# Optimization experiments

Measured on AMD Instinct MI355X. Metric: run time of the kernel, lower is better.

## Reference

```python
import jax, jax.numpy as jnp
import numpy as np

B, C, H, W = 2, 32, 128, 128
K = 5            # window_size
NH = 2           # num_heads
HD = C // NH     # head_dim = 16
KK = K * K
HID = int(2 * C * 2.0)  # mlp hidden = dim*2*mlp_ratio = 128
SCALE = HD ** -0.5


def _ln(x, w, b, eps=1e-5):
    m = jnp.mean(x, -1, keepdims=True)
    v = jnp.var(x, -1, keepdims=True)
    return (x - m) * jax.lax.rsqrt(v + eps) * w + b


def _windows(t):
    # t: [B,H,W,C] -> [B,H,W,C,K*K]; zero-padded KxK neighborhood per pixel
    # (same layout as nn.Unfold: kernel position is the fastest-varying axis).
    p = (K - 1) // 2
    Hc, Wc = t.shape[1], t.shape[2]
    tp = jnp.pad(t, ((0, 0), (p, p), (p, p), (0, 0)))
    return jnp.stack([tp[:, i:i + Hc, j:j + Wc, :] for i in range(K) for j in range(K)], axis=-1)


def _rel_index():
    # Swin-style relative position index for a KxK window -> [KK,KK] ints
    c = jnp.stack(jnp.meshgrid(jnp.arange(K), jnp.arange(K), indexing='ij'), 0).reshape(2, -1)
    r = (c[:, :, None] - c[:, None, :]).transpose(1, 2, 0) + (K - 1)
    return r[..., 0] * (2 * K - 1) + r[..., 1]


def _ckbd_mask(h, w):
    # checkerboard attention mask: [L, KK, KK] additive (0 or -100)
    ck = jnp.zeros((h, w), jnp.float32)
    ck = ck.at[0::2, 1::2].set(1.0).at[1::2, 0::2].set(1.0)
    cw = _windows(ck[None, :, :, None])[0, :, :, 0, :].reshape(h * w, KK)  # [L,KK]
    m = cw[:, :, None] * cw[:, None, :]
    return jnp.where(m == 1.0, 0.0, -100.0)


def setup_inputs() -> dict:
    key = jax.random.key(0)
    ks = jax.random.split(key, 8)
    p = lambda k, s: (0.02 * jax.random.normal(k, s)).astype(jnp.float32)
    return dict(
        x=jax.random.normal(ks[0], (B, C, H, W), dtype=jnp.float32),
        qkv_w=p(ks[1], (3 * C, C)), qkv_b=jnp.zeros((3 * C,), jnp.float32),
        rel_table=p(ks[2], ((2 * K - 1) ** 2, NH)),
        norm1_w=jnp.ones((C,), jnp.float32), norm1_b=jnp.zeros((C,), jnp.float32),
        norm2_w=jnp.ones((2 * C,), jnp.float32), norm2_b=jnp.zeros((2 * C,), jnp.float32),
        proj_w=p(ks[3], (2 * C, 2 * C)), proj_b=jnp.zeros((2 * C,), jnp.float32),
        fusion_w=p(ks[4], (2 * C, C, K, K)), fusion_b=jnp.zeros((2 * C,), jnp.float32),
        mlp_w1=p(ks[5], (HID, 2 * C)), mlp_b1=jnp.zeros((HID,), jnp.float32),
        mlp_w2=p(ks[6], (2 * C, HID)), mlp_b2=jnp.zeros((2 * C,), jnp.float32),
    )


def reference(x, qkv_w, qkv_b, rel_table, norm1_w, norm1_b, norm2_w, norm2_b,
              proj_w, proj_b, fusion_w, fusion_b, mlp_w1, mlp_b1, mlp_w2, mlp_b2):
    Bs, Cs, Hs, Ws = x.shape
    L = Hs * Ws
    xt = x.reshape(Bs, Cs, L).transpose(0, 2, 1)          # [B,L,C]
    xn = _ln(xt, norm1_w, norm1_b)
    qkv = jnp.einsum('blc,oc->blo', xn, qkv_w) + qkv_b     # [B,L,3C]
    qkv = qkv.reshape(Bs, Hs, Ws, 3, Cs)
    q, k, v = qkv[..., 0, :], qkv[..., 1, :], qkv[..., 2, :]  # each [B,H,W,C]

    def heads(t):
        # windows -> [B,L,C,KK]; split C as (head_dim, num_heads) to match the
        # original reshape(B,L,head_dim,num_heads,KK).permute(0,1,3,4,2)
        w_ = _windows(t).reshape(Bs, L, HD, NH, KK)
        return w_.transpose(0, 1, 3, 4, 2)                 # [B,L,nh,KK,hd]

    qh, kh, vh = heads(q), heads(k), heads(v)
    attn = jnp.einsum('blhqd,blhkd->blhqk', qh * SCALE, kh)  # [B,L,nh,KK,KK]

    bias = rel_table[_rel_index().reshape(-1)].reshape(KK, KK, NH).transpose(2, 0, 1)
    attn = attn + bias[None, None]
    attn = attn + _ckbd_mask(Hs, Ws)[None, :, None]
    attn = jax.nn.softmax(attn, axis=-1)

    o = jnp.einsum('blhqk,blhkd->blhqd', attn, vh)           # [B,L,nh,KK,hd]
    # -> [B,L,K,K,nh,hd] -> [B,L,K,K,C] (head-major channel order, as in torch)
    o = o.reshape(Bs, L, NH, K, K, HD).transpose(0, 1, 3, 4, 2, 5).reshape(Bs, L, K, K, Cs)
    # fusion: Conv2d(C, 2C, kernel=K) on [BL,C,K,K] with no padding == full contraction
    y = jnp.einsum('blijc,ocij->blo', o, fusion_w) + fusion_b  # [B,L,2C]
    y = jnp.einsum('blc,oc->blo', y, proj_w) + proj_b
    h1 = _ln(y, norm2_w, norm2_b)
    mlp = jnp.einsum('blh,oh->blo',
                     jax.nn.gelu(jnp.einsum('blc,hc->blh', h1, mlp_w1) + mlp_b1, approximate=False),
                     mlp_w2) + mlp_b2
    y = y + mlp
    return y.transpose(0, 2, 1).reshape(Bs, 2 * Cs, Hs, Ws)
```

## Files before the change

kernel.cpp:

```cpp
#include <hip/hip_runtime.h>
#include <cstdint>
#include <cstddef>

#define HH 128
#define WW 128
#define LL 16384
#define BL 32768

typedef float  f32x4  __attribute__((ext_vector_type(4)));
typedef short  bf16x8 __attribute__((ext_vector_type(8)));
typedef __fp16 h2     __attribute__((ext_vector_type(2)));

union U32H { unsigned u; h2 h; };

static __device__ __forceinline__ float fdot2(h2 a, h2 b, float c) {
  return __builtin_amdgcn_fdot2(a, b, c, false);
}
static __device__ __forceinline__ unsigned pkh2(float a, float b) {
  h2 h = __builtin_amdgcn_cvt_pkrtz(a, b);
  U32H t; t.h = h; return t.u;
}
static __device__ __forceinline__ unsigned short f2bf(float x) {
  union { float f; unsigned int u; } c; c.f = x;
  unsigned int r = (c.u + 0x7fffu + ((c.u >> 16) & 1u)) >> 16;
  return (unsigned short)r;
}

#define LOADH8(dst, ptr) { \
  uint4 _a = *(const uint4*)(ptr); uint4 _b = *(const uint4*)((ptr)+8); U32H _t; \
  _t.u=_a.x; dst[0]=_t.h; _t.u=_a.y; dst[1]=_t.h; _t.u=_a.z; dst[2]=_t.h; _t.u=_a.w; dst[3]=_t.h; \
  _t.u=_b.x; dst[4]=_t.h; _t.u=_b.y; dst[5]=_t.h; _t.u=_b.z; dst[6]=_t.h; _t.u=_b.w; dst[7]=_t.h; }

__global__ __launch_bounds__(256) void k_combine(
    const float* __restrict__ proj_w, const float* __restrict__ proj_b,
    const float* __restrict__ fw, const float* __restrict__ fb,
    const float* __restrict__ w1, const float* __restrict__ w2,
    unsigned short* __restrict__ wctT, float* __restrict__ bc,
    unsigned short* __restrict__ w1b, unsigned short* __restrict__ w2b)
{
  if (blockIdx.x == 200) {
    int o = threadIdx.x;
    if (o < 64) {
      float acc = proj_b[o];
      for (int m = 0; m < 64; ++m) acc = fmaf(proj_w[o*64+m], fb[m], acc);
      bc[o] = acc;
    }
    return;
  }
  if (blockIdx.x == 201) {
    for (int i = threadIdx.x; i < 8192; i += 256) w1b[i] = f2bf(w1[i]);
    return;
  }
  if (blockIdx.x == 202) {
    for (int i = threadIdx.x; i < 8192; i += 256) w2b[i] = f2bf(w2[i]);
    return;
  }
  int gid = blockIdx.x * 256 + threadIdx.x;
  int o  = gid / 800;
  int kk = gid - o * 800;
  int c  = kk & 31;
  int t  = kk >> 5;
  int in = c * 25 + t;
  float acc = 0.f;
  for (int m = 0; m < 64; ++m) acc = fmaf(proj_w[o*64+m], fw[m*800+in], acc);
  wctT[gid] = f2bf(acc);
}

__global__ __launch_bounds__(128) void k_ln_qkv(
    const float* __restrict__ x, const float* __restrict__ qkv_w,
    const float* __restrict__ qkv_b, const float* __restrict__ n1w,
    const float* __restrict__ n1b, unsigned short* __restrict__ qo,
    unsigned short* __restrict__ ko, unsigned short* __restrict__ vo)
{
  __shared__ float sW[32*32];
  __shared__ float sB[32];
  __shared__ float sNw[32], sNb[32];
  int p = blockIdx.y;
  for (int i = threadIdx.x; i < 32*32; i += 128) sW[i] = qkv_w[p*1024 + i];
  if (threadIdx.x < 32) {
    sB[threadIdx.x]  = qkv_b[p*32 + threadIdx.x];
    sNw[threadIdx.x] = n1w[threadIdx.x];
    sNb[threadIdx.x] = n1b[threadIdx.x];
  }
  __syncthreads();
  int gid = blockIdx.x * 128 + threadIdx.x;
  int b = gid >> 14, l = gid & (LL - 1);
  const float* xp = x + (size_t)b * 32 * LL + l;
  float xv[32];
  float mean = 0.f;
  #pragma unroll
  for (int c = 0; c < 32; ++c) { xv[c] = xp[(size_t)c * LL]; mean += xv[c]; }
  mean *= 0.03125f;
  float var = 0.f;
  #pragma unroll
  for (int c = 0; c < 32; ++c) { float d = xv[c] - mean; var = fmaf(d, d, var); }
  float rs = rsqrtf(var * 0.03125f + 1e-5f);
  #pragma unroll
  for (int c = 0; c < 32; ++c) xv[c] = (xv[c] - mean) * rs * sNw[c] + sNb[c];
  float ao[32];
  #pragma unroll
  for (int o = 0; o < 32; ++o) {
    const float* wr = &sW[o * 32];
    float acc = sB[o];
    #pragma unroll
    for (int c = 0; c < 32; ++c) acc = fmaf(xv[c], wr[c], acc);
    ao[(o & 1) * 16 + (o >> 1)] = acc;
  }
  unsigned short* op = (p == 0 ? qo : p == 1 ? ko : vo) + (size_t)gid * 32;
  #pragma unroll
  for (int e = 0; e < 4; ++e) {
    uint4 pk4;
    pk4.x = pkh2(ao[e*8+0], ao[e*8+1]);
    pk4.y = pkh2(ao[e*8+2], ao[e*8+3]);
    pk4.z = pkh2(ao[e*8+4], ao[e*8+5]);
    pk4.w = pkh2(ao[e*8+6], ao[e*8+7]);
    *(uint4*)(op + e*8) = pk4;
  }
}

#define TH 4
#define TW 8
#define NPOS 96
#define KVSTR 40
#define OSTRU 520

__global__ __launch_bounds__(256, 2) void k_attn(
    const unsigned short* __restrict__ qi, const unsigned short* __restrict__ ki,
    const unsigned short* __restrict__ vi, const float* __restrict__ rel_table,
    const unsigned short* __restrict__ wctT, const float* __restrict__ bc,
    float* __restrict__ y2)
{
  __shared__ __align__(16) unsigned short sQ[NPOS*KVSTR];
  __shared__ __align__(16) unsigned short sK[NPOS*KVSTR];
  __shared__ __align__(16) unsigned short sV[NPOS*KVSTR];
  __shared__ __align__(16) unsigned short sO[32*OSTRU];
  __shared__ float sRT[162];
  __shared__ float sPar[NPOS];

  int tid = threadIdx.x;
  int lane = tid & 63, wv = tid >> 6;
  int b  = blockIdx.z;
  int h0 = blockIdx.y * TH, w0 = blockIdx.x * TW;

  for (int i = tid; i < 162; i += 256) sRT[i] = rel_table[i];
  if (tid < NPOS) {
    int ph = tid / 12, pw = tid - ph * 12;
    int h2v = h0 + ph - 2, w2v = w0 + pw - 2;
    bool valid = ((unsigned)h2v < HH) && ((unsigned)w2v < WW);
    sPar[tid] = (valid && (((h2v + w2v) & 1) == 1)) ? 1.f : 0.f;
  }
  for (int idx = tid; idx < 1152; idx += 256) {
    int arr = idx / 384;
    int rem = idx - arr * 384;
    int pos = rem >> 2, c8 = rem & 3;
    int ph = pos / 12, pw = pos - ph * 12;
    int h2v = h0 + ph - 2, w2v = w0 + pw - 2;
    uint4 val = make_uint4(0u, 0u, 0u, 0u);
    if (((unsigned)h2v < HH) && ((unsigned)w2v < WW)) {
      const unsigned short* src = (arr == 0 ? ki : arr == 1 ? vi : qi)
                       + ((size_t)((b << 14) + (h2v << 7) + w2v)) * 32 + c8 * 8;
      val = *(const uint4*)src;
    }
    unsigned short* dp = (arr == 0 ? sK : arr == 1 ? sV : sQ) + pos * KVSTR + c8 * 8;
    *(uint4*)dp = val;
  }
  __syncthreads();

  f32x4 acc[2] = {{0.f,0.f,0.f,0.f},{0.f,0.f,0.f,0.f}};
  int ocol = wv * 16 + (lane & 15);

  for (int it = 0; it < 2; ++it) {
    int g = wv * 2 + (lane >> 5);
    int qd = it * 4 + (g >> 1);
    int nh = g & 1;
    int nh16 = nh * 16;
    if (qd < 7) {
      int nrr = (qd < 6) ? 4 : 1;
      int loc = lane & 31;
      int ly = loc >> 3, lx = loc & 7;
      int posb = ly * 12 + lx;
      int tqb = 4 * qd;
      int tq0 = tqb, tq1 = tqb+1, tq2 = tqb+2, tq3 = tqb+3;
      int iq0 = tq0/5, jq0 = tq0 - iq0*5;
      int iq1 = tq1/5, jq1 = tq1 - iq1*5;
      int iq2 = tq2/5, jq2 = tq2 - iq2*5;
      int iq3 = tq3/5, jq3 = tq3 - iq3*5;
      int pq0 = posb + iq0*12 + jq0; pq0 = pq0 > 95 ? 95 : pq0;
      int pq1 = posb + iq1*12 + jq1; pq1 = pq1 > 95 ? 95 : pq1;
      int pq2 = posb + iq2*12 + jq2; pq2 = pq2 > 95 ? 95 : pq2;
      int pq3 = posb + iq3*12 + jq3; pq3 = pq3 > 95 ? 95 : pq3;
      float parq0 = sPar[pq0], parq1 = sPar[pq1], parq2 = sPar[pq2], parq3 = sPar[pq3];
      h2 q0[8], q1[8], q2[8], q3[8];
      LOADH8(q0, &sQ[pq0*KVSTR + nh16]);
      LOADH8(q1, &sQ[pq1*KVSTR + nh16]);
      LOADH8(q2, &sQ[pq2*KVSTR + nh16]);
      LOADH8(q3, &sQ[pq3*KVSTR + nh16]);
      float s0 = 0.f, s1 = 0.f, s2 = 0.f, s3 = 0.f;
      float oo0[16], oo1[16], oo2[16], oo3[16];
      #pragma unroll
      for (int e = 0; e < 16; ++e) { oo0[e]=0.f; oo1[e]=0.f; oo2[e]=0.f; oo3[e]=0.f; }
      #pragma unroll 1
      for (int ik = 0; ik < 5; ++ik) {
        int rb0 = ((iq0-ik+4)*9 + jq0 + 4)*2 + nh;
        int rb1 = ((iq1-ik+4)*9 + jq1 + 4)*2 + nh;
        int rb2 = ((iq2-ik+4)*9 + jq2 + 4)*2 + nh;
        int rb3 = ((iq3-ik+4)*9 + jq3 + 4)*2 + nh;
        #pragma unroll
        for (int jk = 0; jk < 5; ++jk) {
          int pk = posb + ik*12 + jk;
          h2 kh[8];
          LOADH8(kh, &sK[pk*KVSTR + nh16]);
          float park = sPar[pk];
          float mk = (park == 1.f) ? 0.f : -100.f;
          float a0 = 0.f, a1 = 0.f, a2 = 0.f, a3 = 0.f;
          #pragma unroll
          for (int u = 0; u < 8; ++u) {
            a0 = fdot2(q0[u], kh[u], a0);
            a1 = fdot2(q1[u], kh[u], a1);
            a2 = fdot2(q2[u], kh[u], a2);
            a3 = fdot2(q3[u], kh[u], a3);
          }
          int i0 = rb0 - 2*jk; i0 = i0 > 161 ? 161 : i0;
          int i1 = rb1 - 2*jk; i1 = i1 > 161 ? 161 : i1;
          int i2 = rb2 - 2*jk; i2 = i2 > 161 ? 161 : i2;
          int i3 = rb3 - 2*jk; i3 = i3 > 161 ? 161 : i3;
          float e0 = __expf(fmaf(parq0, mk, fmaf(a0, 0.25f, sRT[i0])));
          float e1 = __expf(fmaf(parq1, mk, fmaf(a1, 0.25f, sRT[i1])));
          float e2 = __expf(fmaf(parq2, mk, fmaf(a2, 0.25f, sRT[i2])));
          float e3 = __expf(fmaf(parq3, mk, fmaf(a3, 0.25f, sRT[i3])));
          s0 += e0; s1 += e1; s2 += e2; s3 += e3;
          h2 vh[8];
          LOADH8(vh, &sV[pk*KVSTR + nh16]);
          #pragma unroll
          for (int u = 0; u < 8; ++u) {
            float lo = (float)vh[u].x, hi = (float)vh[u].y;
            oo0[2*u] = fmaf(e0, lo, oo0[2*u]); oo0[2*u+1] = fmaf(e0, hi, oo0[2*u+1]);
            oo1[2*u] = fmaf(e1, lo, oo1[2*u]); oo1[2*u+1] = fmaf(e1, hi, oo1[2*u+1]);
            oo2[2*u] = fmaf(e2, lo, oo2[2*u]); oo2[2*u+1] = fmaf(e2, hi, oo2[2*u+1]);
            oo3[2*u] = fmaf(e3, lo, oo3[2*u]); oo3[2*u+1] = fmaf(e3, hi, oo3[2*u+1]);
          }
        }
      }
      #define WRITE_ROW(OO, SS, TQ) { \
        float inv = 1.f / (SS); \
        int kl = ((TQ) - it*16) * 32 + nh16; \
        uint4 w4; \
        w4.x = (unsigned)f2bf(OO[0]*inv)  | ((unsigned)f2bf(OO[1]*inv)  << 16); \
        w4.y = (unsigned)f2bf(OO[2]*inv)  | ((unsigned)f2bf(OO[3]*inv)  << 16); \
        w4.z = (unsigned)f2bf(OO[4]*inv)  | ((unsigned)f2bf(OO[5]*inv)  << 16); \
        w4.w = (unsigned)f2bf(OO[6]*inv)  | ((unsigned)f2bf(OO[7]*inv)  << 16); \
        *(uint4*)&sO[loc*OSTRU + kl] = w4; \
        w4.x = (unsigned)f2bf(OO[8]*inv)  | ((unsigned)f2bf(OO[9]*inv)  << 16); \
        w4.y = (unsigned)f2bf(OO[10]*inv) | ((unsigned)f2bf(OO[11]*inv) << 16); \
        w4.z = (unsigned)f2bf(OO[12]*inv) | ((unsigned)f2bf(OO[13]*inv) << 16); \
        w4.w = (unsigned)f2bf(OO[14]*inv) | ((unsigned)f2bf(OO[15]*inv) << 16); \
        *(uint4*)&sO[loc*OSTRU + kl + 8] = w4; }
      WRITE_ROW(oo0, s0, tq0);
      if (1 < nrr) WRITE_ROW(oo1, s1, tq1);
      if (2 < nrr) WRITE_ROW(oo2, s2, tq2);
      if (3 < nrr) WRITE_ROW(oo3, s3, tq3);
      #undef WRITE_ROW
    }
    __syncthreads();
    int ktn = it ? 9 : 16;
    const unsigned short* bcol = wctT + (size_t)ocol * 800 + it * 512 + (lane >> 4) * 8;
    for (int kt = 0; kt < ktn; ++kt) {
      bf16x8 bfrag = *(const bf16x8*)(bcol + kt * 32);
      #pragma unroll
      for (int mt = 0; mt < 2; ++mt) {
        bf16x8 afrag = *(const bf16x8*)&sO[(mt*16 + (lane & 15))*OSTRU + kt*32 + (lane >> 4)*8];
        acc[mt] = __builtin_amdgcn_mfma_f32_16x16x32_bf16(afrag, bfrag, acc[mt], 0, 0, 0);
      }
    }
    __syncthreads();
  }
  float bco = bc[ocol];
  #pragma unroll
  for (int mt = 0; mt < 2; ++mt) {
    #pragma unroll
    for (int r2 = 0; r2 < 4; ++r2) {
      int loc = mt * 16 + (lane >> 4) * 4 + r2;
      int ly = loc >> 3, lx = loc & 7;
      int gid = (b << 14) + ((h0 + ly) << 7) + (w0 + lx);
      y2[(size_t)gid * 64 + ocol] = acc[mt][r2] + bco;
    }
  }
}

__global__ __launch_bounds__(256) void k_mlp(
    const float* __restrict__ y2, const float* __restrict__ n2w,
    const float* __restrict__ n2b, const unsigned short* __restrict__ w1b,
    const float* __restrict__ b1, const unsigned short* __restrict__ w2b,
    const float* __restrict__ b2, float* __restrict__ out)
{
  __shared__ __align__(16) unsigned short sA[64*72];
  __shared__ __align__(16) unsigned short sH[64*136];
  int tid = threadIdx.x;
  int lane = tid & 63, wv = tid >> 6;
  int m0 = blockIdx.x * 64;
  {
    int r = tid >> 2, qd = tid & 3;
    const float* yp = y2 + (size_t)(m0 + r) * 64 + qd * 16;
    float xv[16];
    float s = 0.f;
    #pragma unroll
    for (int e = 0; e < 4; ++e) {
      float4 t4 = *(const float4*)(yp + e*4);
      xv[4*e] = t4.x; xv[4*e+1] = t4.y; xv[4*e+2] = t4.z; xv[4*e+3] = t4.w;
      s += t4.x + t4.y + t4.z + t4.w;
    }
    s += __shfl_xor(s, 1);
    s += __shfl_xor(s, 2);
    float mean = s * (1.f/64.f);
    float v = 0.f;
    #pragma unroll
    for (int e = 0; e < 16; ++e) { float d = xv[e] - mean; v = fmaf(d, d, v); }
    v += __shfl_xor(v, 1);
    v += __shfl_xor(v, 2);
    float rs = rsqrtf(v * (1.f/64.f) + 1e-5f);
    #pragma unroll
    for (int u = 0; u < 8; ++u) {
      int c0 = qd*16 + 2*u;
      float h0v = (xv[2*u]   - mean) * rs * n2w[c0]   + n2b[c0];
      float h1v = (xv[2*u+1] - mean) * rs * n2w[c0+1] + n2b[c0+1];
      *(unsigned*)&sA[r*72 + c0] = (unsigned)f2bf(h0v) | ((unsigned)f2bf(h1v) << 16);
    }
  }
  __syncthreads();
  f32x4 acc1[4][2];
  #pragma unroll
  for (int mt = 0; mt < 4; ++mt)
    #pragma unroll
    for (int nt = 0; nt < 2; ++nt) acc1[mt][nt] = (f32x4){0.f,0.f,0.f,0.f};
  #pragma unroll
  for (int kt = 0; kt < 2; ++kt) {
    #pragma unroll
    for (int nt = 0; nt < 2; ++nt) {
      int ncol = wv*32 + nt*16 + (lane & 15);
      bf16x8 bfrag = *(const bf16x8*)(w1b + ncol*64 + kt*32 + (lane >> 4)*8);
      #pragma unroll
      for (int mt = 0; mt < 4; ++mt) {
        bf16x8 afrag = *(const bf16x8*)&sA[(mt*16 + (lane & 15))*72 + kt*32 + (lane >> 4)*8];
        acc1[mt][nt] = __builtin_amdgcn_mfma_f32_16x16x32_bf16(afrag, bfrag, acc1[mt][nt], 0, 0, 0);
      }
    }
  }
  #pragma unroll
  for (int nt = 0; nt < 2; ++nt) {
    int ncol = wv*32 + nt*16 + (lane & 15);
    float b1v = b1[ncol];
    #pragma unroll
    for (int mt = 0; mt < 4; ++mt) {
      #pragma unroll
      for (int r2 = 0; r2 < 4; ++r2) {
        int mrow = mt*16 + (lane >> 4)*4 + r2;
        float h = acc1[mt][nt][r2] + b1v;
        float g = 0.5f * h * (1.f + erff(h * 0.70710678118f));
        sH[mrow*136 + ncol] = f2bf(g);
      }
    }
  }
  __syncthreads();
  f32x4 acc2[4];
  #pragma unroll
  for (int mt = 0; mt < 4; ++mt) acc2[mt] = (f32x4){0.f,0.f,0.f,0.f};
  int ocol = wv*16 + (lane & 15);
  #pragma unroll
  for (int kt = 0; kt < 4; ++kt) {
    bf16x8 bfrag = *(const bf16x8*)(w2b + ocol*128 + kt*32 + (lane >> 4)*8);
    #pragma unroll
    for (int mt = 0; mt < 4; ++mt) {
      bf16x8 afrag = *(const bf16x8*)&sH[(mt*16 + (lane & 15))*136 + kt*32 + (lane >> 4)*8];
      acc2[mt] = __builtin_amdgcn_mfma_f32_16x16x32_bf16(afrag, bfrag, acc2[mt], 0, 0, 0);
    }
  }
  float b2v = b2[ocol];
  int bb = m0 >> 14;
  #pragma unroll
  for (int mt = 0; mt < 4; ++mt) {
    int mrow = mt*16 + (lane >> 4)*4;
    int l = m0 + mrow;
    const float* yp = y2 + (size_t)l * 64 + ocol;
    float4 o4;
    o4.x = yp[0]   + acc2[mt][0] + b2v;
    o4.y = yp[64]  + acc2[mt][1] + b2v;
    o4.z = yp[128] + acc2[mt][2] + b2v;
    o4.w = yp[192] + acc2[mt][3] + b2v;
    *(float4*)&out[(size_t)bb * 64 * LL + (size_t)ocol * LL + (l - (bb << 14))] = o4;
  }
}

extern "C" void kernel_launch(void* const* d_in, const int* in_sizes, int n_in,
                              void* d_out, int out_size, void* d_ws, size_t ws_size,
                              hipStream_t stream) {
  const float* x         = (const float*)d_in[0];
  const float* qkv_w     = (const float*)d_in[1];
  const float* qkv_b     = (const float*)d_in[2];
  const float* rel_table = (const float*)d_in[3];
  const float* n1w       = (const float*)d_in[4];
  const float* n1b       = (const float*)d_in[5];
  const float* n2w       = (const float*)d_in[6];
  const float* n2b       = (const float*)d_in[7];
  const float* proj_w    = (const float*)d_in[8];
  const float* proj_b    = (const float*)d_in[9];
  const float* fw        = (const float*)d_in[10];
  const float* fb        = (const float*)d_in[11];
  const float* w1        = (const float*)d_in[12];
  const float* b1        = (const float*)d_in[13];
  const float* w2        = (const float*)d_in[14];
  const float* b2        = (const float*)d_in[15];

  char* ws = (char*)d_ws;
  unsigned short* q    = (unsigned short*)(ws);
  unsigned short* k    = (unsigned short*)(ws + 2097152);
  unsigned short* v    = (unsigned short*)(ws + 4194304);
  float*          y2   = (float*)(ws + 6291456);
  unsigned short* wctT = (unsigned short*)(ws + 14680064);
  float*          bc   = (float*)(ws + 14782464);
  unsigned short* w1b  = (unsigned short*)(ws + 14782720);
  unsigned short* w2b  = (unsigned short*)(ws + 14799104);
  float* out = (float*)d_out;

  k_combine<<<203, 256, 0, stream>>>(proj_w, proj_b, fw, fb, w1, w2, wctT, bc, w1b, w2b);
  k_ln_qkv<<<dim3(BL/128, 3), 128, 0, stream>>>(x, qkv_w, qkv_b, n1w, n1b, q, k, v);
  k_attn<<<dim3(WW/TW, HH/TH, 2), 256, 0, stream>>>(q, k, v, rel_table, wctT, bc, y2);
  k_mlp<<<BL/64, 256, 0, stream>>>(y2, n2w, n2b, w1b, b1, w2b, b2, out);
}
```

Baseline: 103.4 us.

## Switch attention and MLP to fp16 packed math and f16 MFMA, split heads in LDS

Measured after the change: 94.29 us. 1.1x faster.

```diff
diff --git a/kernel.cpp b/kernel.cpp
--- a/kernel.cpp
+++ b/kernel.cpp
@@ -8,8 +8,8 @@
 #define BL 32768
 
 typedef float  f32x4  __attribute__((ext_vector_type(4)));
-typedef short  bf16x8 __attribute__((ext_vector_type(8)));
 typedef __fp16 h2     __attribute__((ext_vector_type(2)));
+typedef __fp16 h8     __attribute__((ext_vector_type(8)));
 
 union U32H { unsigned u; h2 h; };
 
@@ -20,10 +20,11 @@
   h2 h = __builtin_amdgcn_cvt_pkrtz(a, b);
   U32H t; t.h = h; return t.u;
 }
-static __device__ __forceinline__ unsigned short f2bf(float x) {
-  union { float f; unsigned int u; } c; c.f = x;
-  unsigned int r = (c.u + 0x7fffu + ((c.u >> 16) & 1u)) >> 16;
-  return (unsigned short)r;
+static __device__ __forceinline__ h2 bcasth(float a) {
+  return __builtin_amdgcn_cvt_pkrtz(a, a);
+}
+static __device__ __forceinline__ unsigned short f2h(float x) {
+  union { __fp16 h; unsigned short u; } c; c.h = (__fp16)x; return c.u;
 }
 
 #define LOADH8(dst, ptr) { \
@@ -36,7 +37,7 @@
     const float* __restrict__ fw, const float* __restrict__ fb,
     const float* __restrict__ w1, const float* __restrict__ w2,
     unsigned short* __restrict__ wctT, float* __restrict__ bc,
-    unsigned short* __restrict__ w1b, unsigned short* __restrict__ w2b)
+    unsigned short* __restrict__ w1h, unsigned short* __restrict__ w2h)
 {
   if (blockIdx.x == 200) {
     int o = threadIdx.x;
@@ -48,11 +49,11 @@
     return;
   }
   if (blockIdx.x == 201) {
-    for (int i = threadIdx.x; i < 8192; i += 256) w1b[i] = f2bf(w1[i]);
+    for (int i = threadIdx.x; i < 8192; i += 256) w1h[i] = f2h(w1[i]);
     return;
   }
   if (blockIdx.x == 202) {
-    for (int i = threadIdx.x; i < 8192; i += 256) w2b[i] = f2bf(w2[i]);
+    for (int i = threadIdx.x; i < 8192; i += 256) w2h[i] = f2h(w2[i]);
     return;
   }
   int gid = blockIdx.x * 256 + threadIdx.x;
@@ -63,7 +64,7 @@
   int in = c * 25 + t;
   float acc = 0.f;
   for (int m = 0; m < 64; ++m) acc = fmaf(proj_w[o*64+m], fw[m*800+in], acc);
-  wctT[gid] = f2bf(acc);
+  wctT[gid] = f2h(acc);
 }
 
 __global__ __launch_bounds__(128) void k_ln_qkv(
@@ -121,18 +122,18 @@
 #define TH 4
 #define TW 8
 #define NPOS 96
-#define KVSTR 40
-#define OSTRU 520
-
-__global__ __launch_bounds__(256, 2) void k_attn(
+#define KVSTR 24
+#define OSTRU 524
+
+__global__ __launch_bounds__(256, 3) void k_attn(
     const unsigned short* __restrict__ qi, const unsigned short* __restrict__ ki,
     const unsigned short* __restrict__ vi, const float* __restrict__ rel_table,
     const unsigned short* __restrict__ wctT, const float* __restrict__ bc,
     float* __restrict__ y2)
 {
-  __shared__ __align__(16) unsigned short sQ[NPOS*KVSTR];
-  __shared__ __align__(16) unsigned short sK[NPOS*KVSTR];
-  __shared__ __align__(16) unsigned short sV[NPOS*KVSTR];
+  __shared__ __align__(16) unsigned short sQ[192*KVSTR];
+  __shared__ __align__(16) unsigned short sK[192*KVSTR];
+  __shared__ __align__(16) unsigned short sV[192*KVSTR];
   __shared__ __align__(16) unsigned short sO[32*OSTRU];
   __shared__ float sRT[162];
   __shared__ float sPar[NPOS];
@@ -152,16 +153,18 @@
   for (int idx = tid; idx < 1152; idx += 256) {
     int arr = idx / 384;
     int rem = idx - arr * 384;
-    int pos = rem >> 2, c8 = rem & 3;
+    int pos = rem >> 2, q4 = rem & 3;
+    int nh = q4 >> 1, half = q4 & 1;
     int ph = pos / 12, pw = pos - ph * 12;
     int h2v = h0 + ph - 2, w2v = w0 + pw - 2;
     uint4 val = make_uint4(0u, 0u, 0u, 0u);
     if (((unsigned)h2v < HH) && ((unsigned)w2v < WW)) {
       const unsigned short* src = (arr == 0 ? ki : arr == 1 ? vi : qi)
-                       + ((size_t)((b << 14) + (h2v << 7) + w2v)) * 32 + c8 * 8;
+                       + ((size_t)((b << 14) + (h2v << 7) + w2v)) * 32 + nh * 16 + half * 8;
       val = *(const uint4*)src;
     }
-    unsigned short* dp = (arr == 0 ? sK : arr == 1 ? sV : sQ) + pos * KVSTR + c8 * 8;
+    unsigned short* dp = (arr == 0 ? sK : arr == 1 ? sV : sQ)
+                       + (nh * 96 + pos) * KVSTR + half * 8;
     *(uint4*)dp = val;
   }
   __syncthreads();
@@ -173,7 +176,7 @@
     int g = wv * 2 + (lane >> 5);
     int qd = it * 4 + (g >> 1);
     int nh = g & 1;
-    int nh16 = nh * 16;
+    int nhb = nh * 96;
     if (qd < 7) {
       int nrr = (qd < 6) ? 4 : 1;
       int loc = lane & 31;
@@ -191,14 +194,17 @@
       int pq3 = posb + iq3*12 + jq3; pq3 = pq3 > 95 ? 95 : pq3;
       float parq0 = sPar[pq0], parq1 = sPar[pq1], parq2 = sPar[pq2], parq3 = sPar[pq3];
       h2 q0[8], q1[8], q2[8], q3[8];
-      LOADH8(q0, &sQ[pq0*KVSTR + nh16]);
-      LOADH8(q1, &sQ[pq1*KVSTR + nh16]);
-      LOADH8(q2, &sQ[pq2*KVSTR + nh16]);
-      LOADH8(q3, &sQ[pq3*KVSTR + nh16]);
+      LOADH8(q0, &sQ[(nhb+pq0)*KVSTR]);
+      LOADH8(q1, &sQ[(nhb+pq1)*KVSTR]);
+      LOADH8(q2, &sQ[(nhb+pq2)*KVSTR]);
+      LOADH8(q3, &sQ[(nhb+pq3)*KVSTR]);
       float s0 = 0.f, s1 = 0.f, s2 = 0.f, s3 = 0.f;
-      float oo0[16], oo1[16], oo2[16], oo3[16];
+      h2 oo0[8], oo1[8], oo2[8], oo3[8];
       #pragma unroll
-      for (int e = 0; e < 16; ++e) { oo0[e]=0.f; oo1[e]=0.f; oo2[e]=0.f; oo3[e]=0.f; }
+      for (int e = 0; e < 8; ++e) {
+        oo0[e] = (h2)(__fp16)0.f; oo1[e] = (h2)(__fp16)0.f;
+        oo2[e] = (h2)(__fp16)0.f; oo3[e] = (h2)(__fp16)0.f;
+      }
       #pragma unroll 1
       for (int ik = 0; ik < 5; ++ik) {
         int rb0 = ((iq0-ik+4)*9 + jq0 + 4)*2 + nh;
@@ -209,7 +215,7 @@
         for (int jk = 0; jk < 5; ++jk) {
           int pk = posb + ik*12 + jk;
           h2 kh[8];
-          LOADH8(kh, &sK[pk*KVSTR + nh16]);
+          LOADH8(kh, &sK[(nhb+pk)*KVSTR]);
           float park = sPar[pk];
           float mk = (park == 1.f) ? 0.f : -100.f;
           float a0 = 0.f, a1 = 0.f, a2 = 0.f, a3 = 0.f;
@@ -229,32 +235,26 @@
           float e2 = __expf(fmaf(parq2, mk, fmaf(a2, 0.25f, sRT[i2])));
           float e3 = __expf(fmaf(parq3, mk, fmaf(a3, 0.25f, sRT[i3])));
           s0 += e0; s1 += e1; s2 += e2; s3 += e3;
+          h2 e0h = bcasth(e0), e1h = bcasth(e1), e2h = bcasth(e2), e3h = bcasth(e3);
           h2 vh[8];
-          LOADH8(vh, &sV[pk*KVSTR + nh16]);
+          LOADH8(vh, &sV[(nhb+pk)*KVSTR]);
           #pragma unroll
           for (int u = 0; u < 8; ++u) {
-            float lo = (float)vh[u].x, hi = (float)vh[u].y;
-            oo0[2*u] = fmaf(e0, lo, oo0[2*u]); oo0[2*u+1] = fmaf(e0, hi, oo0[2*u+1]);
-            oo1[2*u] = fmaf(e1, lo, oo1[2*u]); oo1[2*u+1] = fmaf(e1, hi, oo1[2*u+1]);
-            oo2[2*u] = fmaf(e2, lo, oo2[2*u]); oo2[2*u+1] = fmaf(e2, hi, oo2[2*u+1]);
-            oo3[2*u] = fmaf(e3, lo, oo3[2*u]); oo3[2*u+1] = fmaf(e3, hi, oo3[2*u+1]);
+            oo0[u] = e0h * vh[u] + oo0[u];
+            oo1[u] = e1h * vh[u] + oo1[u];
+            oo2[u] = e2h * vh[u] + oo2[u];
+            oo3[u] = e3h * vh[u] + oo3[u];
           }
         }
       }
       #define WRITE_ROW(OO, SS, TQ) { \
-        float inv = 1.f / (SS); \
-        int kl = ((TQ) - it*16) * 32 + nh16; \
-        uint4 w4; \
-        w4.x = (unsigned)f2bf(OO[0]*inv)  | ((unsigned)f2bf(OO[1]*inv)  << 16); \
-        w4.y = (unsigned)f2bf(OO[2]*inv)  | ((unsigned)f2bf(OO[3]*inv)  << 16); \
-        w4.z = (unsigned)f2bf(OO[4]*inv)  | ((unsigned)f2bf(OO[5]*inv)  << 16); \
-        w4.w = (unsigned)f2bf(OO[6]*inv)  | ((unsigned)f2bf(OO[7]*inv)  << 16); \
-        *(uint4*)&sO[loc*OSTRU + kl] = w4; \
-        w4.x = (unsigned)f2bf(OO[8]*inv)  | ((unsigned)f2bf(OO[9]*inv)  << 16); \
-        w4.y = (unsigned)f2bf(OO[10]*inv) | ((unsigned)f2bf(OO[11]*inv) << 16); \
-        w4.z = (unsigned)f2bf(OO[12]*inv) | ((unsigned)f2bf(OO[13]*inv) << 16); \
-        w4.w = (unsigned)f2bf(OO[14]*inv) | ((unsigned)f2bf(OO[15]*inv) << 16); \
-        *(uint4*)&sO[loc*OSTRU + kl + 8] = w4; }
+        h2 ih = bcasth(1.f / (SS)); \
+        int kl = ((TQ) - it*16) * 32 + nh * 16; \
+        union { h2 h[8]; uint4 u4[2]; } R; \
+        _Pragma("unroll") \
+        for (int u = 0; u < 8; ++u) R.h[u] = OO[u] * ih; \
+        *(uint4*)&sO[loc*OSTRU + kl] = R.u4[0]; \
+        *(uint4*)&sO[loc*OSTRU + kl + 8] = R.u4[1]; }
       WRITE_ROW(oo0, s0, tq0);
       if (1 < nrr) WRITE_ROW(oo1, s1, tq1);
       if (2 < nrr) WRITE_ROW(oo2, s2, tq2);
@@ -265,11 +265,11 @@
     int ktn = it ? 9 : 16;
     const unsigned short* bcol = wctT + (size_t)ocol * 800 + it * 512 + (lane >> 4) * 8;
     for (int kt = 0; kt < ktn; ++kt) {
-      bf16x8 bfrag = *(const bf16x8*)(bcol + kt * 32);
+      h8 bfrag = *(const h8*)(bcol + kt * 32);
       #pragma unroll
       for (int mt = 0; mt < 2; ++mt) {
-        bf16x8 afrag = *(const bf16x8*)&sO[(mt*16 + (lane & 15))*OSTRU + kt*32 + (lane >> 4)*8];
-        acc[mt] = __builtin_amdgcn_mfma_f32_16x16x32_bf16(afrag, bfrag, acc[mt], 0, 0, 0);
+        h8 afrag = *(const h8*)&sO[(mt*16 + (lane & 15))*OSTRU + kt*32 + (lane >> 4)*8];
+        acc[mt] = __builtin_amdgcn_mfma_f32_16x16x32_f16(afrag, bfrag, acc[mt], 0, 0, 0);
       }
     }
     __syncthreads();
@@ -289,8 +289,8 @@
 
 __global__ __launch_bounds__(256) void k_mlp(
     const float* __restrict__ y2, const float* __restrict__ n2w,
-    const float* __restrict__ n2b, const unsigned short* __restrict__ w1b,
-    const float* __restrict__ b1, const unsigned short* __restrict__ w2b,
+    const float* __restrict__ n2b, const unsigned short* __restrict__ w1h,
+    const float* __restrict__ b1, const unsigned short* __restrict__ w2h,
     const float* __restrict__ b2, float* __restrict__ out)
 {
   __shared__ __align__(16) unsigned short sA[64*72];
@@ -323,7 +323,7 @@
       int c0 = qd*16 + 2*u;
       float h0v = (xv[2*u]   - mean) * rs * n2w[c0]   + n2b[c0];
       float h1v = (xv[2*u+1] - mean) * rs * n2w[c0+1] + n2b[c0+1];
-      *(unsigned*)&sA[r*72 + c0] = (unsigned)f2bf(h0v) | ((unsigned)f2bf(h1v) << 16);
+      *(unsigned*)&sA[r*72 + c0] = pkh2(h0v, h1v);
     }
   }
   __syncthreads();
@@ -337,11 +337,11 @@
     #pragma unroll
     for (int nt = 0; nt < 2; ++nt) {
       int ncol = wv*32 + nt*16 + (lane & 15);
-      bf16x8 bfrag = *(const bf16x8*)(w1b + ncol*64 + kt*32 + (lane >> 4)*8);
+      h8 bfrag = *(const h8*)(w1h + ncol*64 + kt*32 + (lane >> 4)*8);
       #pragma unroll
       for (int mt = 0; mt < 4; ++mt) {
-        bf16x8 afrag = *(const bf16x8*)&sA[(mt*16 + (lane & 15))*72 + kt*32 + (lane >> 4)*8];
-        acc1[mt][nt] = __builtin_amdgcn_mfma_f32_16x16x32_bf16(afrag, bfrag, acc1[mt][nt], 0, 0, 0);
+        h8 afrag = *(const h8*)&sA[(mt*16 + (lane & 15))*72 + kt*32 + (lane >> 4)*8];
+        acc1[mt][nt] = __builtin_amdgcn_mfma_f32_16x16x32_f16(afrag, bfrag, acc1[mt][nt], 0, 0, 0);
       }
     }
   }
@@ -356,7 +356,7 @@
         int mrow = mt*16 + (lane >> 4)*4 + r2;
         float h = acc1[mt][nt][r2] + b1v;
         float g = 0.5f * h * (1.f + erff(h * 0.70710678118f));
-        sH[mrow*136 + ncol] = f2bf(g);
+        sH[mrow*136 + ncol] = f2h(g);
       }
     }
   }
@@ -367,11 +367,11 @@
   int ocol = wv*16 + (lane & 15);
   #pragma unroll
   for (int kt = 0; kt < 4; ++kt) {
-    bf16x8 bfrag = *(const bf16x8*)(w2b + ocol*128 + kt*32 + (lane >> 4)*8);
+    h8 bfrag = *(const h8*)(w2h + ocol*128 + kt*32 + (lane >> 4)*8);
     #pragma unroll
     for (int mt = 0; mt < 4; ++mt) {
-      bf16x8 afrag = *(const bf16x8*)&sH[(mt*16 + (lane & 15))*136 + kt*32 + (lane >> 4)*8];
-      acc2[mt] = __builtin_amdgcn_mfma_f32_16x16x32_bf16(afrag, bfrag, acc2[mt], 0, 0, 0);
+      h8 afrag = *(const h8*)&sH[(mt*16 + (lane & 15))*136 + kt*32 + (lane >> 4)*8];
+      acc2[mt] = __builtin_amdgcn_mfma_f32_16x16x32_f16(afrag, bfrag, acc2[mt], 0, 0, 0);
     }
   }
   float b2v = b2[ocol];
@@ -417,12 +417,12 @@
   float*          y2   = (float*)(ws + 6291456);
   unsigned short* wctT = (unsigned short*)(ws + 14680064);
   float*          bc   = (float*)(ws + 14782464);
-  unsigned short* w1b  = (unsigned short*)(ws + 14782720);
-  unsigned short* w2b  = (unsigned short*)(ws + 14799104);
+  unsigned short* w1h  = (unsigned short*)(ws + 14782720);
+  unsigned short* w2h  = (unsigned short*)(ws + 14799104);
   float* out = (float*)d_out;
 
-  k_combine<<<203, 256, 0, stream>>>(proj_w, proj_b, fw, fb, w1, w2, wctT, bc, w1b, w2b);
+  k_combine<<<203, 256, 0, stream>>>(proj_w, proj_b, fw, fb, w1, w2, wctT, bc, w1h, w2h);
   k_ln_qkv<<<dim3(BL/128, 3), 128, 0, stream>>>(x, qkv_w, qkv_b, n1w, n1b, q, k, v);
   k_attn<<<dim3(WW/TW, HH/TH, 2), 256, 0, stream>>>(q, k, v, rel_table, wctT, bc, y2);
-  k_mlp<<<BL/64, 256, 0, stream>>>(y2, n2w, n2b, w1b, b1, w2b, b2, out);
-}
+  k_mlp<<<BL/64, 256, 0, stream>>>(y2, n2w, n2b, w1h, b1, w2h, b2, out);
+}
```
